# Kernel tuning notes

Hardware: AMD Instinct MI355X
Metric: run time of the kernel (lower is better)

The kernel has to match this reference:

```python
import jax, jax.numpy as jnp
import numpy as np

IN_FEATURES = 4096
OUT_FEATURES = 16384

def setup_inputs() -> dict:
    key = jax.random.key(0)
    k1, k2 = jax.random.split(key)
    x = jax.random.normal(k1, (4, 2048, IN_FEATURES), dtype=jnp.float32)
    # init_weights: uniform(-1, 1)
    W = jax.random.uniform(k2, (OUT_FEATURES, IN_FEATURES), dtype=jnp.float32, minval=-1.0, maxval=1.0)
    b = jnp.zeros((OUT_FEATURES,), dtype=jnp.float32)
    return {"x": x, "W": W, "b": b}

def reference(x, W, b):
    # Binarize weights to {-1, 0, +1} via sign, then dense linear: y = x @ sign(W)^T + b
    Wb = jnp.sign(W)
    return jnp.einsum('bsd,od->bso', x, Wb) + b
```

## Files before the change

### kernel.cpp

```cpp
#include <hip/hip_runtime.h>
#include <hip/hip_bf16.h>

#define M_TOT 8192
#define N_TOT 16384
#define K_TOT 4096
#define BM 128
#define BN 256
#define BK 64
#define NT (K_TOT / BK)

typedef int i32x4 __attribute__((ext_vector_type(4)));
typedef int i32x16 __attribute__((ext_vector_type(16)));
typedef __bf16 bf16x8 __attribute__((ext_vector_type(8)));
typedef float f32x4 __attribute__((ext_vector_type(4)));

#define GLOAD_LDS16(g, l)                                                     \
  __builtin_amdgcn_global_load_lds(                                           \
      (__attribute__((address_space(1))) const void*)(g),                     \
      (__attribute__((address_space(3))) void*)(l), 16, 0, 0)

__device__ __forceinline__ ushort f2bf_rne(float f) {
  unsigned u = __float_as_uint(f);
  u += 0x7FFFu + ((u >> 16) & 1u);
  return (ushort)(u >> 16);
}
__device__ __forceinline__ ushort sgn_bf16(float w) {
  return w > 0.f ? (ushort)0x3F80u : (w < 0.f ? (ushort)0xBF80u : (ushort)0u);
}

__global__ void quant_x_kernel(const float* __restrict__ x,
                               char* __restrict__ xq, float* __restrict__ s) {
  int row = blockIdx.x;
  const float4* xr = (const float4*)(x + (size_t)row * K_TOT);
  int tid = threadIdx.x;
  float4 v[4];
  float amax = 0.f;
#pragma unroll
  for (int j = 0; j < 4; ++j) {
    v[j] = xr[j * 256 + tid];
    amax = fmaxf(amax, fmaxf(fmaxf(fabsf(v[j].x), fabsf(v[j].y)),
                             fmaxf(fabsf(v[j].z), fabsf(v[j].w))));
  }
#pragma unroll
  for (int o = 32; o > 0; o >>= 1) amax = fmaxf(amax, __shfl_xor(amax, o));
  __shared__ float wmax[4];
  if ((tid & 63) == 0) wmax[tid >> 6] = amax;
  __syncthreads();
  amax = fmaxf(fmaxf(wmax[0], wmax[1]), fmaxf(wmax[2], wmax[3]));
  float inv = amax > 0.f ? 127.0f / amax : 0.f;
  if (tid == 0) s[row] = amax * (1.0f / 127.0f);
  int* out = (int*)(xq + (size_t)row * K_TOT);
#pragma unroll
  for (int j = 0; j < 4; ++j) {
    int q0 = max(-127, min(127, __float2int_rn(v[j].x * inv)));
    int q1 = max(-127, min(127, __float2int_rn(v[j].y * inv)));
    int q2 = max(-127, min(127, __float2int_rn(v[j].z * inv)));
    int q3 = max(-127, min(127, __float2int_rn(v[j].w * inv)));
    out[j * 256 + tid] =
        (q0 & 255) | ((q1 & 255) << 8) | ((q2 & 255) << 16) | ((q3 & 255) << 24);
  }
}

__global__ void quant_w_kernel(const float* __restrict__ w,
                               char* __restrict__ wq, int n4) {
  int i = blockIdx.x * blockDim.x + threadIdx.x;
  int stride = gridDim.x * blockDim.x;
  for (; i < n4; i += stride) {
    float4 v = ((const float4*)w)[i];
    int q0 = v.x > 0.f ? 1 : (v.x < 0.f ? -1 : 0);
    int q1 = v.y > 0.f ? 1 : (v.y < 0.f ? -1 : 0);
    int q2 = v.z > 0.f ? 1 : (v.z < 0.f ? -1 : 0);
    int q3 = v.w > 0.f ? 1 : (v.w < 0.f ? -1 : 0);
    ((int*)wq)[i] =
        (q0 & 255) | ((q1 & 255) << 8) | ((q2 & 255) << 16) | ((q3 & 255) << 24);
  }
}

__global__ __launch_bounds__(512, 4) void gemm_i8_dual(
    const char* __restrict__ A, const char* __restrict__ B,
    const float* __restrict__ s, const float* __restrict__ bias,
    float* __restrict__ C) {
  __shared__ char ldsA[2][128 * 64];
  __shared__ char ldsB[2][256 * 64];

  int bid = blockIdx.x;
  int wg = (bid & 7) * 512 + (bid >> 3);
  int bnSup = wg >> 9;
  int rem = wg & 511;
  int bm = rem >> 3;
  int bn = bnSup * 8 + (rem & 7);
  int rowBase = bm * BM;
  int colBase = bn * BN;

  int t = threadIdx.x;
  int lane = t & 63;
  int wave = t >> 6;
  int wr = wave >> 2;
  int wc = wave & 3;
  int l31 = lane & 31;
  int hi = lane >> 5;

  int sc = ((t & 3) ^ ((t >> 3) & 3)) * 16;
  const char* gA = A + (size_t)(rowBase + (t >> 2)) * K_TOT + sc;
  const char* gB0 = B + (size_t)(colBase + (t >> 2)) * K_TOT + sc;
  const char* gB1 = gB0 + (size_t)128 * K_TOT;
  int lt = t * 16;

  int rxor = (l31 >> 1) & 3;
  int cs0 = (hi ^ rxor) * 16;
  int cs1 = ((2 | hi) ^ rxor) * 16;
  int arow = (wr * 64 + l31) * 64;
  int brow = (wc * 64 + l31) * 64;

  i32x16 acc[2][2] = {};

#define STAGE(kt_, buf_)                                                      \
  {                                                                           \
    size_t _o = (size_t)(kt_)*64;                                             \
    GLOAD_LDS16(gA + _o, &ldsA[buf_][lt]);                                    \
    GLOAD_LDS16(gB0 + _o, &ldsB[buf_][lt]);                                   \
    GLOAD_LDS16(gB1 + _o, &ldsB[buf_][8192 + lt]);                            \
  }

  STAGE(0, 0);
  STAGE(1, 1);
  asm volatile("s_waitcnt vmcnt(3)" ::: "memory");
  __builtin_amdgcn_s_barrier();

  for (int tt = 0; tt < NT; ++tt) {
    int b = tt & 1;
    const char* la = &ldsA[b][0];
    const char* lb = &ldsB[b][0];
    i32x4 af[2], bf[2];
    af[0] = *(const i32x4*)(la + arow + cs0);
    af[1] = *(const i32x4*)(la + arow + 2048 + cs0);
    bf[0] = *(const i32x4*)(lb + brow + cs0);
    bf[1] = *(const i32x4*)(lb + brow + 2048 + cs0);
    __builtin_amdgcn_s_setprio(1);
#pragma unroll
    for (int mi = 0; mi < 2; ++mi)
#pragma unroll
      for (int ni = 0; ni < 2; ++ni)
        acc[mi][ni] = __builtin_amdgcn_mfma_i32_32x32x32_i8(af[mi], bf[ni],
                                                            acc[mi][ni], 0, 0, 0);
    __builtin_amdgcn_s_setprio(0);
    af[0] = *(const i32x4*)(la + arow + cs1);
    af[1] = *(const i32x4*)(la + arow + 2048 + cs1);
    bf[0] = *(const i32x4*)(lb + brow + cs1);
    bf[1] = *(const i32x4*)(lb + brow + 2048 + cs1);
    __builtin_amdgcn_s_setprio(1);
#pragma unroll
    for (int mi = 0; mi < 2; ++mi)
#pragma unroll
      for (int ni = 0; ni < 2; ++ni)
        acc[mi][ni] = __builtin_amdgcn_mfma_i32_32x32x32_i8(af[mi], bf[ni],
                                                            acc[mi][ni], 0, 0, 0);
    __builtin_amdgcn_s_setprio(0);

    __builtin_amdgcn_s_barrier();
    if (tt + 2 < NT) {
      STAGE(tt + 2, b);
      asm volatile("s_waitcnt vmcnt(3)" ::: "memory");
    } else if (tt + 1 < NT) {
      asm volatile("s_waitcnt vmcnt(0)" ::: "memory");
    }
    __builtin_amdgcn_s_barrier();
  }

#undef STAGE

#pragma unroll
  for (int mi = 0; mi < 2; ++mi) {
#pragma unroll
    for (int ni = 0; ni < 2; ++ni) {
      int gc = colBase + wc * 64 + ni * 32 + l31;
      float bv = bias[gc];
#pragma unroll
      for (int rg = 0; rg < 16; ++rg) {
        int rowIn = (rg & 3) + 8 * (rg >> 2) + 4 * hi;
        int gr = rowBase + wr * 64 + mi * 32 + rowIn;
        C[(size_t)gr * N_TOT + gc] = (float)acc[mi][ni][rg] * s[gr] + bv;
      }
    }
  }
}

__global__ void gemm_fused_kernel(const float* __restrict__ A,
                                  const float* __restrict__ W,
                                  const float* __restrict__ bias,
                                  float* __restrict__ C) {
  __shared__ ushort lsA[128 * 32];
  __shared__ ushort lsB[128 * 32];

  int nwg = gridDim.x;
  int bid = blockIdx.x;
  int wg = (bid & 7) * (nwg >> 3) + (bid >> 3);
  const int NBN = N_TOT / 128;
  int bm = wg / NBN;
  int bn = wg % NBN;
  int rowBase = bm * 128;
  int colBase = bn * 128;

  int t = threadIdx.x;
  int lane = t & 63;
  int wave = t >> 6;
  int wm = (wave >> 1) * 64;
  int wn = (wave & 1) * 64;

  f32x4 acc[4][4] = {};

  int srow = t >> 3;
  int scol = (t & 7) * 4;
  int fr = lane & 15;
  int koff = (lane >> 4) * 8;

  for (int k0 = 0; k0 < K_TOT; k0 += 32) {
    float4 va[4], vb[4];
#pragma unroll
    for (int r = 0; r < 4; ++r) {
      va[r] = *(const float4*)&A[(size_t)(rowBase + r * 32 + srow) * K_TOT + k0 + scol];
      vb[r] = *(const float4*)&W[(size_t)(colBase + r * 32 + srow) * K_TOT + k0 + scol];
    }
    __syncthreads();
#pragma unroll
    for (int r = 0; r < 4; ++r) {
      int e = r * 1024 + t * 4;
      ushort4 oa, ob;
      oa.x = f2bf_rne(va[r].x); oa.y = f2bf_rne(va[r].y);
      oa.z = f2bf_rne(va[r].z); oa.w = f2bf_rne(va[r].w);
      ob.x = sgn_bf16(vb[r].x); ob.y = sgn_bf16(vb[r].y);
      ob.z = sgn_bf16(vb[r].z); ob.w = sgn_bf16(vb[r].w);
      *(ushort4*)&lsA[e] = oa;
      *(ushort4*)&lsB[e] = ob;
    }
    __syncthreads();

    bf16x8 af[4], bfr[4];
#pragma unroll
    for (int i = 0; i < 4; ++i)
      af[i] = *(const bf16x8*)&lsA[(wm + i * 16 + fr) * 32 + koff];
#pragma unroll
    for (int j = 0; j < 4; ++j)
      bfr[j] = *(const bf16x8*)&lsB[(wn + j * 16 + fr) * 32 + koff];

#pragma unroll
    for (int i = 0; i < 4; ++i)
#pragma unroll
      for (int j = 0; j < 4; ++j)
        acc[i][j] = __builtin_amdgcn_mfma_f32_16x16x32_bf16(af[i], bfr[j],
                                                            acc[i][j], 0, 0, 0);
  }

  int orow0 = rowBase + wm + ((lane >> 4) << 2);
  int ocol0 = colBase + wn + (lane & 15);
#pragma unroll
  for (int i = 0; i < 4; ++i) {
#pragma unroll
    for (int j = 0; j < 4; ++j) {
      int col = ocol0 + j * 16;
      float bv = bias[col];
#pragma unroll
      for (int rg = 0; rg < 4; ++rg) {
        int row = orow0 + i * 16 + rg;
        C[(size_t)row * N_TOT + col] = acc[i][j][rg] + bv;
      }
    }
  }
}

extern "C" void kernel_launch(void* const* d_in, const int* in_sizes, int n_in,
                              void* d_out, int out_size, void* d_ws,
                              size_t ws_size, hipStream_t stream) {
  const float* x = (const float*)d_in[0];
  const float* W = (const float*)d_in[1];
  const float* b = (const float*)d_in[2];
  float* out = (float*)d_out;

  const size_t xq_bytes = (size_t)M_TOT * K_TOT;
  const size_t wq_bytes = (size_t)N_TOT * K_TOT;
  const size_t need = xq_bytes + wq_bytes + M_TOT * 4;

  if (ws_size >= need) {
    char* xq = (char*)d_ws;
    char* wq = xq + xq_bytes;
    float* s = (float*)(wq + wq_bytes);
    quant_x_kernel<<<M_TOT, 256, 0, stream>>>(x, xq, s);
    quant_w_kernel<<<2048, 256, 0, stream>>>(W, wq, (int)(wq_bytes / 4));
    const int nblocks = (M_TOT / BM) * (N_TOT / BN);
    gemm_i8_dual<<<nblocks, 512, 0, stream>>>(xq, wq, s, b, out);
  } else {
    const int nblocks = (M_TOT / 128) * (N_TOT / 128);
    gemm_fused_kernel<<<nblocks, 256, 0, stream>>>(x, W, b, out);
  }
}
```

Measured before the change: 782.8 us.

## Restructure int8 GEMM to 256x128 tile, 4 waves, triple-buffered LDS

Switches the int8 GEMM from a 128x256 tile with 8 waves and double buffering to a 256x128 tile with 4 waves, each computing a 128x64 sub-tile (4x2 MFMAs per k-slice). LDS becomes a three-stage ring, so the prefetch for step tt+2 is issued before compute and only one barrier per iteration remains. The LDS layout is re-swizzled into 32-row, 16-byte-chunk blocks. The aim is more MFMA work per LDS fragment load and better overlap of global loads with compute. The cost is more accumulator registers per thread (128 i32), which limits occupancy.

After: 825.2 us. 5.4% more time.

```diff
diff --git a/kernel.cpp b/kernel.cpp
--- a/kernel.cpp
+++ b/kernel.cpp
@@ -4,8 +4,8 @@
 #define M_TOT 8192
 #define N_TOT 16384
 #define K_TOT 4096
-#define BM 128
-#define BN 256
+#define BM 256
+#define BN 128
 #define BK 64
 #define NT (K_TOT / BK)
 
@@ -76,101 +76,113 @@
   }
 }
 
-__global__ __launch_bounds__(512, 4) void gemm_i8_dual(
+__global__ __launch_bounds__(256, 2) void gemm_i8_tri(
     const char* __restrict__ A, const char* __restrict__ B,
     const float* __restrict__ s, const float* __restrict__ bias,
     float* __restrict__ C) {
-  __shared__ char ldsA[2][128 * 64];
-  __shared__ char ldsB[2][256 * 64];
+  __shared__ char lds[3][24576];
 
   int bid = blockIdx.x;
   int wg = (bid & 7) * 512 + (bid >> 3);
-  int bnSup = wg >> 9;
+  int bnS = wg >> 9;
   int rem = wg & 511;
-  int bm = rem >> 3;
-  int bn = bnSup * 8 + (rem & 7);
+  int bm = rem >> 4;
+  int bn = bnS * 16 + (rem & 15);
   int rowBase = bm * BM;
   int colBase = bn * BN;
 
   int t = threadIdx.x;
   int lane = t & 63;
   int wave = t >> 6;
-  int wr = wave >> 2;
-  int wc = wave & 3;
+  int wr = wave >> 1;
+  int wc = wave & 1;
   int l31 = lane & 31;
   int hi = lane >> 5;
 
-  int sc = ((t & 3) ^ ((t >> 3) & 3)) * 16;
-  const char* gA = A + (size_t)(rowBase + (t >> 2)) * K_TOT + sc;
-  const char* gB0 = B + (size_t)(colBase + (t >> 2)) * K_TOT + sc;
-  const char* gB1 = gB0 + (size_t)128 * K_TOT;
-  int lt = t * 16;
-
-  int rxor = (l31 >> 1) & 3;
-  int cs0 = (hi ^ rxor) * 16;
-  int cs1 = ((2 | hi) ^ rxor) * 16;
-  int arow = (wr * 64 + l31) * 64;
-  int brow = (wc * 64 + l31) * 64;
-
-  i32x16 acc[2][2] = {};
+  const char* gAp[4];
+#pragma unroll
+  for (int q = 0; q < 4; ++q) {
+    int sA = t + 256 * q;
+    int ksA = (sA >> 9) & 1, rgA = (sA >> 6) & 7;
+    int j = sA & 63;
+    int vrow = j >> 2;
+    int craw = (j & 3) ^ ((j >> 3) & 3);
+    int rA = rgA * 32 + vrow + ((craw & 1) << 4);
+    int kA = ksA * 32 + ((craw >> 1) << 4);
+    gAp[q] = A + (size_t)(rowBase + rA) * K_TOT + kA;
+  }
+  const char* gBp[2];
+#pragma unroll
+  for (int q = 0; q < 2; ++q) {
+    int sB = t + 256 * q;
+    int ksB = (sB >> 8) & 1, rgB = (sB >> 6) & 3;
+    int j = sB & 63;
+    int vrow = j >> 2;
+    int craw = (j & 3) ^ ((j >> 3) & 3);
+    int rB = rgB * 32 + vrow + ((craw & 1) << 4);
+    int kB = ksB * 32 + ((craw >> 1) << 4);
+    gBp[q] = B + (size_t)(colBase + rB) * K_TOT + kB;
+  }
+
+  int inb = ((((l31 & 15) << 2) |
+              (((l31 >> 4) | (hi << 1)) ^ ((l31 >> 1) & 3)))) << 4;
+
+  i32x16 acc[4][2] = {};
 
 #define STAGE(kt_, buf_)                                                      \
   {                                                                           \
     size_t _o = (size_t)(kt_)*64;                                             \
-    GLOAD_LDS16(gA + _o, &ldsA[buf_][lt]);                                    \
-    GLOAD_LDS16(gB0 + _o, &ldsB[buf_][lt]);                                   \
-    GLOAD_LDS16(gB1 + _o, &ldsB[buf_][8192 + lt]);                            \
+    char* _d = &lds[buf_][0];                                                 \
+    GLOAD_LDS16(gAp[0] + _o, _d + t * 16);                                    \
+    GLOAD_LDS16(gAp[1] + _o, _d + 4096 + t * 16);                             \
+    GLOAD_LDS16(gAp[2] + _o, _d + 8192 + t * 16);                             \
+    GLOAD_LDS16(gAp[3] + _o, _d + 12288 + t * 16);                            \
+    GLOAD_LDS16(gBp[0] + _o, _d + 16384 + t * 16);                            \
+    GLOAD_LDS16(gBp[1] + _o, _d + 20480 + t * 16);                            \
   }
 
   STAGE(0, 0);
   STAGE(1, 1);
-  asm volatile("s_waitcnt vmcnt(3)" ::: "memory");
+  asm volatile("s_waitcnt vmcnt(6)" ::: "memory");
   __builtin_amdgcn_s_barrier();
 
+  int cur = 0;
   for (int tt = 0; tt < NT; ++tt) {
-    int b = tt & 1;
-    const char* la = &ldsA[b][0];
-    const char* lb = &ldsB[b][0];
-    i32x4 af[2], bf[2];
-    af[0] = *(const i32x4*)(la + arow + cs0);
-    af[1] = *(const i32x4*)(la + arow + 2048 + cs0);
-    bf[0] = *(const i32x4*)(lb + brow + cs0);
-    bf[1] = *(const i32x4*)(lb + brow + 2048 + cs0);
-    __builtin_amdgcn_s_setprio(1);
-#pragma unroll
-    for (int mi = 0; mi < 2; ++mi)
+    int n2 = cur + 2 >= 3 ? cur - 1 : cur + 2;
+    if (tt + 2 < NT) STAGE(tt + 2, n2);
+    const char* la = &lds[cur][0];
+    const char* lb = la + 16384;
+    i32x4 af[4], bf[2];
+#pragma unroll
+    for (int ks = 0; ks < 2; ++ks) {
+#pragma unroll
+      for (int mi = 0; mi < 4; ++mi)
+        af[mi] = *(const i32x4*)(la + ((ks * 8 + wr * 4 + mi) << 10) + inb);
 #pragma unroll
       for (int ni = 0; ni < 2; ++ni)
-        acc[mi][ni] = __builtin_amdgcn_mfma_i32_32x32x32_i8(af[mi], bf[ni],
-                                                            acc[mi][ni], 0, 0, 0);
-    __builtin_amdgcn_s_setprio(0);
-    af[0] = *(const i32x4*)(la + arow + cs1);
-    af[1] = *(const i32x4*)(la + arow + 2048 + cs1);
-    bf[0] = *(const i32x4*)(lb + brow + cs1);
-    bf[1] = *(const i32x4*)(lb + brow + 2048 + cs1);
-    __builtin_amdgcn_s_setprio(1);
-#pragma unroll
-    for (int mi = 0; mi < 2; ++mi)
-#pragma unroll
-      for (int ni = 0; ni < 2; ++ni)
-        acc[mi][ni] = __builtin_amdgcn_mfma_i32_32x32x32_i8(af[mi], bf[ni],
-                                                            acc[mi][ni], 0, 0, 0);
-    __builtin_amdgcn_s_setprio(0);
-
-    __builtin_amdgcn_s_barrier();
+        bf[ni] = *(const i32x4*)(lb + ((ks * 4 + wc * 2 + ni) << 10) + inb);
+      __builtin_amdgcn_s_setprio(1);
+#pragma unroll
+      for (int mi = 0; mi < 4; ++mi)
+#pragma unroll
+        for (int ni = 0; ni < 2; ++ni)
+          acc[mi][ni] = __builtin_amdgcn_mfma_i32_32x32x32_i8(
+              af[mi], bf[ni], acc[mi][ni], 0, 0, 0);
+      __builtin_amdgcn_s_setprio(0);
+    }
     if (tt + 2 < NT) {
-      STAGE(tt + 2, b);
-      asm volatile("s_waitcnt vmcnt(3)" ::: "memory");
+      asm volatile("s_waitcnt vmcnt(6)" ::: "memory");
     } else if (tt + 1 < NT) {
       asm volatile("s_waitcnt vmcnt(0)" ::: "memory");
     }
     __builtin_amdgcn_s_barrier();
+    cur = cur == 2 ? 0 : cur + 1;
   }
 
 #undef STAGE
 
 #pragma unroll
-  for (int mi = 0; mi < 2; ++mi) {
+  for (int mi = 0; mi < 4; ++mi) {
 #pragma unroll
     for (int ni = 0; ni < 2; ++ni) {
       int gc = colBase + wc * 64 + ni * 32 + l31;
@@ -178,7 +190,7 @@
 #pragma unroll
       for (int rg = 0; rg < 16; ++rg) {
         int rowIn = (rg & 3) + 8 * (rg >> 2) + 4 * hi;
-        int gr = rowBase + wr * 64 + mi * 32 + rowIn;
+        int gr = rowBase + wr * 128 + mi * 32 + rowIn;
         C[(size_t)gr * N_TOT + gc] = (float)acc[mi][ni][rg] * s[gr] + bv;
       }
     }
@@ -287,7 +299,7 @@
     quant_x_kernel<<<M_TOT, 256, 0, stream>>>(x, xq, s);
     quant_w_kernel<<<2048, 256, 0, stream>>>(W, wq, (int)(wq_bytes / 4));
     const int nblocks = (M_TOT / BM) * (N_TOT / BN);
-    gemm_i8_dual<<<nblocks, 512, 0, stream>>>(xq, wq, s, b, out);
+    gemm_i8_tri<<<nblocks, 256, 0, stream>>>(xq, wq, s, b, out);
   } else {
     const int nblocks = (M_TOT / 128) * (N_TOT / 128);
     gemm_fused_kernel<<<nblocks, 256, 0, stream>>>(x, W, b, out);
```

## Triple-buffer LDS in int8 GEMM and issue prefetch before compute with one barrier

Applied to the files above, without the earlier changes.

Replaces the double-buffered A/B shared tiles with a three-slot ring. The tile two steps ahead is now issued at the start of each iteration, before the MFMA work, which removes one of the two barriers per K step. The global-to-LDS mapping is rearranged into 32-row by 16-byte swizzled sub-blocks so each wave reads its fragments with a single precomputed offset. All fragments are loaded up front instead of in two halves, and the setprio hints are dropped. The cost is more LDS per block (72 KB versus 48 KB), which may reduce how many blocks fit on a CU.

After: 813.0 us. 1.04x slower.

```diff
diff --git a/kernel.cpp b/kernel.cpp
--- a/kernel.cpp
+++ b/kernel.cpp
@@ -76,19 +76,18 @@
   }
 }
 
-__global__ __launch_bounds__(512, 4) void gemm_i8_dual(
+__global__ __launch_bounds__(512, 4) void gemm_i8_tri16(
     const char* __restrict__ A, const char* __restrict__ B,
     const float* __restrict__ s, const float* __restrict__ bias,
     float* __restrict__ C) {
-  __shared__ char ldsA[2][128 * 64];
-  __shared__ char ldsB[2][256 * 64];
+  __shared__ char lds[3][24576];
 
   int bid = blockIdx.x;
   int wg = (bid & 7) * 512 + (bid >> 3);
-  int bnSup = wg >> 9;
+  int bnS = wg >> 9;
   int rem = wg & 511;
   int bm = rem >> 3;
-  int bn = bnSup * 8 + (rem & 7);
+  int bn = bnS * 8 + (rem & 7);
   int rowBase = bm * BM;
   int colBase = bn * BN;
 
@@ -100,26 +99,31 @@
   int l31 = lane & 31;
   int hi = lane >> 5;
 
-  int sc = ((t & 3) ^ ((t >> 3) & 3)) * 16;
-  const char* gA = A + (size_t)(rowBase + (t >> 2)) * K_TOT + sc;
-  const char* gB0 = B + (size_t)(colBase + (t >> 2)) * K_TOT + sc;
-  const char* gB1 = gB0 + (size_t)128 * K_TOT;
-  int lt = t * 16;
-
-  int rxor = (l31 >> 1) & 3;
-  int cs0 = (hi ^ rxor) * 16;
-  int cs1 = ((2 | hi) ^ rxor) * 16;
-  int arow = (wr * 64 + l31) * 64;
-  int brow = (wc * 64 + l31) * 64;
+  {
+  }
+  int jA = t & 63;
+  int vrowA = jA >> 2;
+  int crawA = (jA & 3) ^ ((jA >> 3) & 3);
+  int rA = ((t >> 6) & 3) * 32 + vrowA + ((crawA & 1) << 4);
+  int kA = ((t >> 8) & 1) * 32 + ((crawA >> 1) << 4);
+  const char* gA = A + (size_t)(rowBase + rA) * K_TOT + kA;
+  int rB = ((t >> 6) & 7) * 32 + vrowA + ((crawA & 1) << 4);
+  int kB = (crawA >> 1) << 4;
+  const char* gB0 = B + (size_t)(colBase + rB) * K_TOT + kB;
+  const char* gB1 = gB0 + 32;
+
+  int inb = ((((l31 & 15) << 2) |
+              (((l31 >> 4) | (hi << 1)) ^ ((l31 >> 1) & 3)))) << 4;
 
   i32x16 acc[2][2] = {};
 
 #define STAGE(kt_, buf_)                                                      \
   {                                                                           \
     size_t _o = (size_t)(kt_)*64;                                             \
-    GLOAD_LDS16(gA + _o, &ldsA[buf_][lt]);                                    \
-    GLOAD_LDS16(gB0 + _o, &ldsB[buf_][lt]);                                   \
-    GLOAD_LDS16(gB1 + _o, &ldsB[buf_][8192 + lt]);                            \
+    char* _d = &lds[buf_][0];                                                 \
+    GLOAD_LDS16(gA + _o, _d + t * 16);                                        \
+    GLOAD_LDS16(gB0 + _o, _d + 8192 + t * 16);                                \
+    GLOAD_LDS16(gB1 + _o, _d + 16384 + t * 16);                               \
   }
 
   STAGE(0, 0);
@@ -127,44 +131,43 @@
   asm volatile("s_waitcnt vmcnt(3)" ::: "memory");
   __builtin_amdgcn_s_barrier();
 
+  int cur = 0;
   for (int tt = 0; tt < NT; ++tt) {
-    int b = tt & 1;
-    const char* la = &ldsA[b][0];
-    const char* lb = &ldsB[b][0];
-    i32x4 af[2], bf[2];
-    af[0] = *(const i32x4*)(la + arow + cs0);
-    af[1] = *(const i32x4*)(la + arow + 2048 + cs0);
-    bf[0] = *(const i32x4*)(lb + brow + cs0);
-    bf[1] = *(const i32x4*)(lb + brow + 2048 + cs0);
-    __builtin_amdgcn_s_setprio(1);
+    int n2 = cur + 2 >= 3 ? cur - 1 : cur + 2;
+    if (tt + 2 < NT) STAGE(tt + 2, n2);
+    const char* la = &lds[cur][0];
+    i32x4 a0[2], b0[2], a1[2], b1[2];
+#pragma unroll
+    for (int mi = 0; mi < 2; ++mi)
+      a0[mi] = *(const i32x4*)(la + ((wr * 2 + mi) << 10) + inb);
+#pragma unroll
+    for (int ni = 0; ni < 2; ++ni)
+      b0[ni] = *(const i32x4*)(la + 8192 + ((wc * 2 + ni) << 10) + inb);
+#pragma unroll
+    for (int mi = 0; mi < 2; ++mi)
+      a1[mi] = *(const i32x4*)(la + ((4 + wr * 2 + mi) << 10) + inb);
+#pragma unroll
+    for (int ni = 0; ni < 2; ++ni)
+      b1[ni] = *(const i32x4*)(la + 8192 + ((8 + wc * 2 + ni) << 10) + inb);
 #pragma unroll
     for (int mi = 0; mi < 2; ++mi)
 #pragma unroll
       for (int ni = 0; ni < 2; ++ni)
-        acc[mi][ni] = __builtin_amdgcn_mfma_i32_32x32x32_i8(af[mi], bf[ni],
+        acc[mi][ni] = __builtin_amdgcn_mfma_i32_32x32x32_i8(a0[mi], b0[ni],
                                                             acc[mi][ni], 0, 0, 0);
-    __builtin_amdgcn_s_setprio(0);
-    af[0] = *(const i32x4*)(la + arow + cs1);
-    af[1] = *(const i32x4*)(la + arow + 2048 + cs1);
-    bf[0] = *(const i32x4*)(lb + brow + cs1);
-    bf[1] = *(const i32x4*)(lb + brow + 2048 + cs1);
-    __builtin_amdgcn_s_setprio(1);
 #pragma unroll
     for (int mi = 0; mi < 2; ++mi)
 #pragma unroll
       for (int ni = 0; ni < 2; ++ni)
-        acc[mi][ni] = __builtin_amdgcn_mfma_i32_32x32x32_i8(af[mi], bf[ni],
+        acc[mi][ni] = __builtin_amdgcn_mfma_i32_32x32x32_i8(a1[mi], b1[ni],
                                                             acc[mi][ni], 0, 0, 0);
-    __builtin_amdgcn_s_setprio(0);
-
-    __builtin_amdgcn_s_barrier();
     if (tt + 2 < NT) {
-      STAGE(tt + 2, b);
       asm volatile("s_waitcnt vmcnt(3)" ::: "memory");
     } else if (tt + 1 < NT) {
       asm volatile("s_waitcnt vmcnt(0)" ::: "memory");
     }
     __builtin_amdgcn_s_barrier();
+    cur = cur == 2 ? 0 : cur + 1;
   }
 
 #undef STAGE
@@ -287,7 +290,7 @@
     quant_x_kernel<<<M_TOT, 256, 0, stream>>>(x, xq, s);
     quant_w_kernel<<<2048, 256, 0, stream>>>(W, wq, (int)(wq_bytes / 4));
     const int nblocks = (M_TOT / BM) * (N_TOT / BN);
-    gemm_i8_dual<<<nblocks, 512, 0, stream>>>(xq, wq, s, b, out);
+    gemm_i8_tri16<<<nblocks, 512, 0, stream>>>(xq, wq, s, b, out);
   } else {
     const int nblocks = (M_TOT / 128) * (N_TOT / 128);
     gemm_fused_kernel<<<nblocks, 256, 0, stream>>>(x, W, b, out);
```
